# Kernel optimization log

Measured on AMD Instinct MI355X. Metric: run time of the kernel, lower is better.

## Reference

```python
import jax, jax.numpy as jnp
import numpy as np

N_QUMODES = 128
N_LAYERS = 8
BATCH = 131072
HBAR = 2.0  # PennyLane default.gaussian convention; vacuum covariance = I


def setup_inputs() -> dict:
    key = jax.random.key(0)
    k1, k2 = jax.random.split(key)
    inputs = jax.random.normal(k1, (BATCH, N_QUMODES), dtype=jnp.float32)
    params = jax.random.normal(k2, (N_LAYERS, 3 * N_QUMODES), dtype=jnp.float32)
    return {"inputs": inputs, "params": params}


def _rot(theta):
    # Rotation gate on (x, p): x -> c x - s p, p -> s x + c p. Shape [..., 2, 2].
    c, s = jnp.cos(theta), jnp.sin(theta)
    return jnp.stack([jnp.stack([c, -s], -1), jnp.stack([s, c], -1)], -2)


def _build_symplectic(params):
    """Compose the full 2N x 2N symplectic matrix for all layers.

    Per layer: local per-mode blocks R(th2) @ Sq(r) @ R(th1), then a fixed
    chain of pi/4 beamsplitters on modes (0,1),(1,2),...  Quadrature ordering
    is interleaved: (x0, p0, x1, p1, ...).
    """
    N, L = N_QUMODES, N_LAYERS
    p = params.reshape(L, N, 3)
    th1, r, th2 = p[..., 0], p[..., 1], p[..., 2]
    z = jnp.zeros_like(r)
    sq = jnp.stack([jnp.stack([jnp.exp(-r), z], -1),
                    jnp.stack([z, jnp.exp(r)], -1)], -2)  # [L, N, 2, 2]
    blk = jnp.einsum('lnab,lnbc,lncd->lnad', _rot(th2), sq, _rot(th1))

    # Fixed beamsplitter chain matrix C (theta = pi/4, phi = 0).
    t = float(np.cos(np.pi / 4))
    rr = float(np.sin(np.pi / 4))
    BS4 = jnp.array([[t, 0., -rr, 0.],
                     [0., t, 0., -rr],
                     [rr, 0., t, 0.],
                     [0., rr, 0., t]], dtype=params.dtype)
    C = jnp.eye(2 * N, dtype=params.dtype)
    for i in range(N - 1):
        C = C.at[2 * i:2 * i + 4, :].set(BS4 @ C[2 * i:2 * i + 4, :])

    idx = jnp.arange(N)
    S = jnp.eye(2 * N, dtype=params.dtype)
    for l in range(L):
        D = jnp.zeros((N, 2, N, 2), params.dtype).at[idx, :, idx, :].set(blk[l])
        S = C @ (D.reshape(2 * N, 2 * N) @ S)
    return S


def reference(inputs, params):
    """Batched Gaussian simulation of the CV QNN; returns <n_i> per sample."""
    S = _build_symplectic(params)
    B, N = inputs.shape[0], N_QUMODES
    # Displacement(a, 0): mu_x += sqrt(2*hbar) * a = 2a for hbar = 2.
    mu0 = jnp.zeros((B, 2 * N), inputs.dtype).at[:, 0::2].set(2.0 * inputs)
    mu = mu0 @ S.T                      # [B, 2N]
    V = S @ S.T                         # vacuum cov = I -> V = S S^T
    dV = jnp.diagonal(V)
    dsum = dV[0::2] + dV[1::2]          # V_xx + V_pp per mode, [N]
    n = (dsum[None, :] + mu[:, 0::2] ** 2 + mu[:, 1::2] ** 2) / (2.0 * HBAR) - 0.5
    return n
```

## Files before the change

kernel.cpp:

```cpp
#include <hip/hip_runtime.h>


#define BATCH 131072
#define PSTR 40

typedef __attribute__((ext_vector_type(8))) short bf16x8;
typedef __attribute__((ext_vector_type(4))) float f32x4;

#define MFMA(a, b, c) __builtin_amdgcn_mfma_f32_16x16x32_bf16(a, b, c, 0, 0, 0)

__device__ __forceinline__ unsigned short f2bf(float f) {
  unsigned int u = __float_as_uint(f);
  u += 0x7FFFu + ((u >> 16) & 1u);
  return (unsigned short)(u >> 16);
}
__device__ __forceinline__ float bf2f(unsigned short h) {
  return __uint_as_float(((unsigned int)h) << 16);
}
__device__ __forceinline__ void pack8(const float* v, uint4& hv, uint4& lv) {
  unsigned int hw[4], lw[4];
#pragma unroll
  for (int p = 0; p < 4; ++p) {
    unsigned short h0 = f2bf(v[2 * p]), h1 = f2bf(v[2 * p + 1]);
    unsigned short l0 = f2bf(v[2 * p] - bf2f(h0)), l1 = f2bf(v[2 * p + 1] - bf2f(h1));
    hw[p] = (unsigned int)h0 | ((unsigned int)h1 << 16);
    lw[p] = (unsigned int)l0 | ((unsigned int)l1 << 16);
  }
  hv = make_uint4(hw[0], hw[1], hw[2], hw[3]);
  lv = make_uint4(lw[0], lw[1], lw[2], lw[3]);
}

__device__ __forceinline__ float cxf(const float* powc, int a, int nn) {
  if (a < 127) {
    if (nn == 0) return powc[a + 1];
    if (nn <= a) return powc[a - nn + 2];
    if (nn == a + 1) return -0.70710678118654752f;
    return 0.0f;
  }
  return (nn == 0) ? powc[127] : powc[128 - nn];
}

__global__ __launch_bounds__(256) void l1_prod(const float* __restrict__ params,
                                               unsigned short* __restrict__ Phi,
                                               unsigned short* __restrict__ Plo) {
  __shared__ __align__(16) char lds_raw[4 * 128 * PSTR * 2];
  __shared__ float blkA[128][4];
  __shared__ float blkB[128][4];
  __shared__ float powc[132];
  unsigned short* sLhi = (unsigned short*)lds_raw;
  unsigned short* sLlo = sLhi + 128 * PSTR;
  unsigned short* sRhi = sLlo + 128 * PSTR;
  unsigned short* sRlo = sRhi + 128 * PSTR;
  float* sEp = (float*)lds_raw;

  int bx = blockIdx.x;
  int pair = bx >> 2, tile = bx & 3;
  int tr = tile >> 1, tc = tile & 1;
  int t = threadIdx.x;
  int lane = t & 63, w = t >> 6;
  int wr = (w >> 1) * 64, wc = (w & 1) * 64;
  int l15 = lane & 15, q = lane >> 4;

  {
    int l = (t < 128) ? (2 * pair + 1) : (2 * pair);
    int nn = t & 127;
    const float* p = params + l * 384 + nn * 3;
    float th1 = p[0], r = p[1], th2 = p[2];
    float c1 = cosf(th1), s1 = sinf(th1);
    float c2 = cosf(th2), s2 = sinf(th2);
    float em = expf(-r), ep = expf(r);
    float* dst = (t < 128) ? blkA[nn] : blkB[nn];
    dst[0] = c2 * c1 * em - s2 * s1 * ep;
    dst[1] = -c2 * s1 * em - s2 * c1 * ep;
    dst[2] = s2 * c1 * em + c2 * s1 * ep;
    dst[3] = -s2 * s1 * em + c2 * c1 * ep;
    if (t < 132) powc[t] = exp2f(-0.5f * (float)t);
  }

  f32x4 acc[4][4];
#pragma unroll
  for (int a = 0; a < 4; ++a)
#pragma unroll
    for (int b = 0; b < 4; ++b) acc[a][b] = (f32x4){0.f, 0.f, 0.f, 0.f};

  for (int kc = 0; kc < 256; kc += 32) {
    __syncthreads();
#pragma unroll
    for (int it = 0; it < 2; ++it) {
      int e = it * 2048 + t * 8;
      int row = e >> 5, k0 = e & 31;
      {
        int i = tr * 128 + row;
        int a = i >> 1;
        float vv[8];
#pragma unroll
        for (int jj = 0; jj < 8; ++jj) {
          int j = kc + k0 + jj;
          int nn = j >> 1;
          vv[jj] = cxf(powc, a, nn) * blkA[nn][(i & 1) * 2 + (j & 1)];
        }
        uint4 hv, lv;
        pack8(vv, hv, lv);
        *(uint4*)(sLhi + row * PSTR + k0) = hv;
        *(uint4*)(sLlo + row * PSTR + k0) = lv;
      }
      {
        int j = tc * 128 + row;
        int nn = j >> 1;
        float b0 = blkB[nn][0 + (j & 1)];
        float b1 = blkB[nn][2 + (j & 1)];
        float vv[8];
#pragma unroll
        for (int jj = 0; jj < 8; ++jj) {
          int i = kc + k0 + jj;
          vv[jj] = cxf(powc, i >> 1, nn) * ((i & 1) ? b1 : b0);
        }
        uint4 hv, lv;
        pack8(vv, hv, lv);
        *(uint4*)(sRhi + row * PSTR + k0) = hv;
        *(uint4*)(sRlo + row * PSTR + k0) = lv;
      }
    }
    __syncthreads();
    int kb = q * 8;
    bf16x8 afh[4], afl[4], bfh[4], bfl[4];
#pragma unroll
    for (int rt = 0; rt < 4; ++rt) {
      int r = wr + rt * 16 + l15;
      afh[rt] = *(const bf16x8*)(sLhi + r * PSTR + kb);
      afl[rt] = *(const bf16x8*)(sLlo + r * PSTR + kb);
      int n = wc + rt * 16 + l15;
      bfh[rt] = *(const bf16x8*)(sRhi + n * PSTR + kb);
      bfl[rt] = *(const bf16x8*)(sRlo + n * PSTR + kb);
    }
#pragma unroll
    for (int rt = 0; rt < 4; ++rt)
#pragma unroll
      for (int ct = 0; ct < 4; ++ct) {
        acc[rt][ct] = MFMA(afh[rt], bfh[ct], acc[rt][ct]);
        acc[rt][ct] = MFMA(afh[rt], bfl[ct], acc[rt][ct]);
        acc[rt][ct] = MFMA(afl[rt], bfh[ct], acc[rt][ct]);
      }
  }

  for (int ph = 0; ph < 2; ++ph) {
    __syncthreads();
    if (wr == ph * 64) {
#pragma unroll
      for (int rt = 0; rt < 4; ++rt)
#pragma unroll
        for (int ct = 0; ct < 4; ++ct) {
          int rl = rt * 16 + q * 4;
          int col = wc + ct * 16 + l15;
#pragma unroll
          for (int rg = 0; rg < 4; ++rg) sEp[(rl + rg) * 129 + col] = acc[rt][ct][rg];
        }
    }
    __syncthreads();
    if (pair & 1) {
      int rl = t >> 2, cseg = (t & 3) * 32;
      for (int cc = 0; cc < 32; cc += 8) {
        float v[8];
#pragma unroll
        for (int jj = 0; jj < 8; ++jj) v[jj] = sEp[rl * 129 + cseg + cc + jj];
        uint4 hv, lv;
        pack8(v, hv, lv);
        int off = pair * 65536 + (tr * 128 + ph * 64 + rl) * 256 + tc * 128 + cseg + cc;
        *(uint4*)(Phi + off) = hv;
        *(uint4*)(Plo + off) = lv;
      }
    } else {
      int col = t >> 1, rseg = (t & 1) * 32;
      for (int cc = 0; cc < 32; cc += 8) {
        float v[8];
#pragma unroll
        for (int jj = 0; jj < 8; ++jj) v[jj] = sEp[(rseg + cc + jj) * 129 + col];
        uint4 hv, lv;
        pack8(v, hv, lv);
        int off = pair * 65536 + (tc * 128 + col) * 256 + tr * 128 + ph * 64 + rseg + cc;
        *(uint4*)(Phi + off) = hv;
        *(uint4*)(Plo + off) = lv;
      }
    }
  }
}

__global__ __launch_bounds__(256) void matprod(
    const unsigned short* __restrict__ Lhi_base, const unsigned short* __restrict__ Llo_base,
    unsigned short* __restrict__ Ohi, unsigned short* __restrict__ Olo) {
  __shared__ __align__(16) char lds_raw[4 * 128 * PSTR * 2];
  unsigned short* sLhi = (unsigned short*)lds_raw;
  unsigned short* sLlo = sLhi + 128 * PSTR;
  unsigned short* sRhi = sLlo + 128 * PSTR;
  unsigned short* sRlo = sRhi + 128 * PSTR;
  float* sEp = (float*)lds_raw;

  int bx = blockIdx.x;
  int pair = bx >> 2, tile = bx & 3;
  int tr = tile >> 1, tc = tile & 1;
  const unsigned short* Lhi = Lhi_base + (2 * pair + 1) * 65536;
  const unsigned short* Llo = Llo_base + (2 * pair + 1) * 65536;
  const unsigned short* Rhi = Lhi_base + (2 * pair) * 65536;
  const unsigned short* Rlo = Llo_base + (2 * pair) * 65536;

  int t = threadIdx.x;
  int lane = t & 63, w = t >> 6;
  int wr = (w >> 1) * 64, wc = (w & 1) * 64;
  int l15 = lane & 15, q = lane >> 4;

  f32x4 acc[4][4];
#pragma unroll
  for (int a = 0; a < 4; ++a)
#pragma unroll
    for (int b = 0; b < 4; ++b) acc[a][b] = (f32x4){0.f, 0.f, 0.f, 0.f};

  for (int kc = 0; kc < 256; kc += 32) {
    __syncthreads();
#pragma unroll
    for (int it = 0; it < 2; ++it) {
      int e = it * 2048 + t * 8;
      int row = e >> 5, k = e & 31;
      *(uint4*)(sLhi + row * PSTR + k) = *(const uint4*)(Lhi + (tr * 128 + row) * 256 + kc + k);
      *(uint4*)(sLlo + row * PSTR + k) = *(const uint4*)(Llo + (tr * 128 + row) * 256 + kc + k);
      *(uint4*)(sRhi + row * PSTR + k) = *(const uint4*)(Rhi + (tc * 128 + row) * 256 + kc + k);
      *(uint4*)(sRlo + row * PSTR + k) = *(const uint4*)(Rlo + (tc * 128 + row) * 256 + kc + k);
    }
    __syncthreads();
    int kb = q * 8;
    bf16x8 afh[4], afl[4], bfh[4], bfl[4];
#pragma unroll
    for (int rt = 0; rt < 4; ++rt) {
      int r = wr + rt * 16 + l15;
      afh[rt] = *(const bf16x8*)(sLhi + r * PSTR + kb);
      afl[rt] = *(const bf16x8*)(sLlo + r * PSTR + kb);
      int n = wc + rt * 16 + l15;
      bfh[rt] = *(const bf16x8*)(sRhi + n * PSTR + kb);
      bfl[rt] = *(const bf16x8*)(sRlo + n * PSTR + kb);
    }
#pragma unroll
    for (int rt = 0; rt < 4; ++rt)
#pragma unroll
      for (int ct = 0; ct < 4; ++ct) {
        acc[rt][ct] = MFMA(afh[rt], bfh[ct], acc[rt][ct]);
        acc[rt][ct] = MFMA(afh[rt], bfl[ct], acc[rt][ct]);
        acc[rt][ct] = MFMA(afl[rt], bfh[ct], acc[rt][ct]);
      }
  }

  for (int ph = 0; ph < 2; ++ph) {
    __syncthreads();
    if (wr == ph * 64) {
#pragma unroll
      for (int rt = 0; rt < 4; ++rt)
#pragma unroll
        for (int ct = 0; ct < 4; ++ct) {
          int rl = rt * 16 + q * 4;
          int col = wc + ct * 16 + l15;
#pragma unroll
          for (int rg = 0; rg < 4; ++rg) sEp[(rl + rg) * 129 + col] = acc[rt][ct][rg];
        }
    }
    __syncthreads();
    if (pair & 1) {
      int rl = t >> 2, cseg = (t & 3) * 32;
      for (int cc = 0; cc < 32; cc += 8) {
        float v[8];
#pragma unroll
        for (int jj = 0; jj < 8; ++jj) v[jj] = sEp[rl * 129 + cseg + cc + jj];
        uint4 hv, lv;
        pack8(v, hv, lv);
        int off = pair * 65536 + (tr * 128 + ph * 64 + rl) * 256 + tc * 128 + cseg + cc;
        *(uint4*)(Ohi + off) = hv;
        *(uint4*)(Olo + off) = lv;
      }
    } else {
      int col = t >> 1, rseg = (t & 1) * 32;
      for (int cc = 0; cc < 32; cc += 8) {
        float v[8];
#pragma unroll
        for (int jj = 0; jj < 8; ++jj) v[jj] = sEp[(rseg + cc + jj) * 129 + col];
        uint4 hv, lv;
        pack8(v, hv, lv);
        int off = pair * 65536 + (tc * 128 + col) * 256 + tr * 128 + ph * 64 + rseg + cc;
        *(uint4*)(Ohi + off) = hv;
        *(uint4*)(Olo + off) = lv;
      }
    }
  }
}

__global__ __launch_bounds__(256) void l3_fused(
    const unsigned short* __restrict__ Qhi, const unsigned short* __restrict__ Qlo,
    unsigned short* __restrict__ Wb, float* __restrict__ dsum_part) {
  __shared__ __align__(16) char lds_raw[4 * 128 * PSTR * 2];
  unsigned short* sLhi = (unsigned short*)lds_raw;
  unsigned short* sLlo = sLhi + 128 * PSTR;
  unsigned short* sRhi = sLlo + 128 * PSTR;
  unsigned short* sRlo = sRhi + 128 * PSTR;
  float* sEp = (float*)lds_raw;

  int tile = blockIdx.x & 3;
  int tr = tile >> 1, tc = tile & 1;
  const unsigned short* Lhi = Qhi + 65536;
  const unsigned short* Llo = Qlo + 65536;
  const unsigned short* Rhi = Qhi;
  const unsigned short* Rlo = Qlo;

  int t = threadIdx.x;
  int lane = t & 63, w = t >> 6;
  int wr = (w >> 1) * 64, wc = (w & 1) * 64;
  int l15 = lane & 15, q = lane >> 4;

  f32x4 acc[4][4];
#pragma unroll
  for (int a = 0; a < 4; ++a)
#pragma unroll
    for (int b = 0; b < 4; ++b) acc[a][b] = (f32x4){0.f, 0.f, 0.f, 0.f};

  for (int kc = 0; kc < 256; kc += 32) {
    __syncthreads();
#pragma unroll
    for (int it = 0; it < 2; ++it) {
      int e = it * 2048 + t * 8;
      int row = e >> 5, k = e & 31;
      *(uint4*)(sLhi + row * PSTR + k) = *(const uint4*)(Lhi + (tr * 128 + row) * 256 + kc + k);
      *(uint4*)(sLlo + row * PSTR + k) = *(const uint4*)(Llo + (tr * 128 + row) * 256 + kc + k);
      *(uint4*)(sRhi + row * PSTR + k) = *(const uint4*)(Rhi + (tc * 128 + row) * 256 + kc + k);
      *(uint4*)(sRlo + row * PSTR + k) = *(const uint4*)(Rlo + (tc * 128 + row) * 256 + kc + k);
    }
    __syncthreads();
    int kb = q * 8;
    bf16x8 afh[4], afl[4], bfh[4], bfl[4];
#pragma unroll
    for (int rt = 0; rt < 4; ++rt) {
      int r = wr + rt * 16 + l15;
      afh[rt] = *(const bf16x8*)(sLhi + r * PSTR + kb);
      afl[rt] = *(const bf16x8*)(sLlo + r * PSTR + kb);
      int n = wc + rt * 16 + l15;
      bfh[rt] = *(const bf16x8*)(sRhi + n * PSTR + kb);
      bfl[rt] = *(const bf16x8*)(sRlo + n * PSTR + kb);
    }
#pragma unroll
    for (int rt = 0; rt < 4; ++rt)
#pragma unroll
      for (int ct = 0; ct < 4; ++ct) {
        acc[rt][ct] = MFMA(afh[rt], bfh[ct], acc[rt][ct]);
        acc[rt][ct] = MFMA(afh[rt], bfl[ct], acc[rt][ct]);
        acc[rt][ct] = MFMA(afl[rt], bfh[ct], acc[rt][ct]);
      }
  }

  for (int ph = 0; ph < 2; ++ph) {
    __syncthreads();
    if (wr == ph * 64) {
#pragma unroll
      for (int rt = 0; rt < 4; ++rt)
#pragma unroll
        for (int ct = 0; ct < 4; ++ct) {
          int rl = rt * 16 + q * 4;
          int col = wc + ct * 16 + l15;
#pragma unroll
          for (int rg = 0; rg < 4; ++rg) sEp[(rl + rg) * 129 + col] = acc[rt][ct][rg];
        }
    }
    __syncthreads();
    int rbase = tr * 128 + ph * 64;
    int ctbase = tr * 4 + ph * 2;
#pragma unroll
    for (int ci = 0; ci < 2; ++ci) {
      int cell = w * 2 + ci;
      int c2 = cell >> 1;
      int ct = ctbase + (c2 & 1) + ((c2 & 2) ? 8 : 0);
      int ks = 2 * tc + (cell & 1);
      int n = ct * 16 + l15;
      int srow = (n < 128) ? (2 * n) : (2 * (n - 128) + 1);
      int lr = srow - rbase;
      int lc0 = (cell & 1) * 64 + q * 16;
      float v[8];
#pragma unroll
      for (int jj = 0; jj < 8; ++jj) v[jj] = 2.0f * sEp[lr * 129 + lc0 + 2 * jj];
      unsigned int wd[4];
#pragma unroll
      for (int p2 = 0; p2 < 4; ++p2)
        wd[p2] = (unsigned int)f2bf(v[2 * p2]) | ((unsigned int)f2bf(v[2 * p2 + 1]) << 16);
      *(uint4*)(Wb + ((ct * 4 + ks) * 64 + lane) * 8) = make_uint4(wd[0], wd[1], wd[2], wd[3]);
    }
    {
      int ii = t >> 3, s = t & 7;
      int c0 = s * 16;
      float sum = 0.f;
#pragma unroll
      for (int c = 0; c < 16; ++c) {
        float x = sEp[(2 * ii) * 129 + c0 + c];
        float y = sEp[(2 * ii + 1) * 129 + c0 + c];
        sum += x * x + y * y;
      }
      sum += __shfl_down(sum, 4, 8);
      sum += __shfl_down(sum, 2, 8);
      sum += __shfl_down(sum, 1, 8);
      if (s == 0) dsum_part[tc * 128 + (rbase >> 1) + ii] = sum;
    }
  }
}

__global__ __launch_bounds__(256) void qnn_gemm(
    const float* __restrict__ A, const unsigned short* __restrict__ Wb,
    const float* __restrict__ dsum_part, float* __restrict__ out) {
  __shared__ unsigned short sA[64 * 136];
  int t = threadIdx.x;
  int lane = t & 63, w = t >> 6;
  int wr = w >> 1, wc = w & 1;
  int l15 = lane & 15, q = lane >> 4;
  long brow0 = (long)blockIdx.x * 64;

#pragma unroll
  for (int it = 0; it < 8; ++it) {
    int e = it * 1024 + t * 4;
    int row = e >> 7, k = e & 127;
    f32x4 v = __builtin_nontemporal_load((const f32x4*)(A + brow0 * 128 + e));
    *(uint2*)(sA + row * 136 + k) = make_uint2(
        (unsigned int)f2bf(v.x) | ((unsigned int)f2bf(v.y) << 16),
        (unsigned int)f2bf(v.z) | ((unsigned int)f2bf(v.w) << 16));
  }
  __syncthreads();

  f32x4 acc[2][4][2];
#pragma unroll
  for (int rt = 0; rt < 2; ++rt)
#pragma unroll
    for (int qq = 0; qq < 4; ++qq)
#pragma unroll
      for (int xp = 0; xp < 2; ++xp) acc[rt][qq][xp] = (f32x4){0.f, 0.f, 0.f, 0.f};

#pragma unroll
  for (int ks = 0; ks < 4; ++ks) {
    int kb = ks * 32 + q * 8;
    bf16x8 a0 = *(const bf16x8*)(sA + (wr * 32 + l15) * 136 + kb);
    bf16x8 a1 = *(const bf16x8*)(sA + (wr * 32 + 16 + l15) * 136 + kb);
#pragma unroll
    for (int qq = 0; qq < 4; ++qq)
#pragma unroll
      for (int xp = 0; xp < 2; ++xp) {
        int ct = wc * 4 + qq + 8 * xp;
        bf16x8 b = *(const bf16x8*)(Wb + ((ct * 4 + ks) * 64 + lane) * 8);
        acc[0][qq][xp] = MFMA(a0, b, acc[0][qq][xp]);
        acc[1][qq][xp] = MFMA(a1, b, acc[1][qq][xp]);
      }
  }

#pragma unroll
  for (int qq = 0; qq < 4; ++qq) {
    int i = (wc * 4 + qq) * 16 + l15;
    float ds = dsum_part[i] + dsum_part[128 + i];
#pragma unroll
    for (int rt = 0; rt < 2; ++rt) {
      long row0 = brow0 + wr * 32 + rt * 16 + q * 4;
      f32x4 ax = acc[rt][qq][0];
      f32x4 ap = acc[rt][qq][1];
#pragma unroll
      for (int rg = 0; rg < 4; ++rg) {
        float val = 0.25f * (ds + ax[rg] * ax[rg] + ap[rg] * ap[rg]) - 0.5f;
        __builtin_nontemporal_store(val, &out[(row0 + rg) * 128 + i]);
      }
    }
  }
}

extern "C" void kernel_launch(void* const* d_in, const int* in_sizes, int n_in,
                              void* d_out, int out_size, void* d_ws, size_t ws_size,
                              hipStream_t stream) {
  const float* inputs = (const float*)d_in[0];
  const float* params = (const float*)d_in[1];
  float* out = (float*)d_out;

  unsigned short* Phi = (unsigned short*)d_ws;
  unsigned short* Plo = Phi + 4 * 65536;
  unsigned short* Qhi = Plo + 4 * 65536;
  unsigned short* Qlo = Qhi + 2 * 65536;
  unsigned short* Wb = Qlo + 2 * 65536;
  float* dsum_part = (float*)(Wb + 65536);

  l1_prod<<<16, 256, 0, stream>>>(params, Phi, Plo);
  matprod<<<8, 256, 0, stream>>>(Phi, Plo, Qhi, Qlo);
  l3_fused<<<4, 256, 0, stream>>>(Qhi, Qlo, Wb, dsum_part);
  qnn_gemm<<<2048, 256, 0, stream>>>(inputs, Wb, dsum_part, out);
}
```

Before: 184.2 us.

## Make GEMM blocks persistent over four row chunks with register-prefetched double buffer

Each block of the batched GEMM now processes four 64-row chunks instead of one. The next chunk's fp32 inputs are loaded into registers while the current chunk's MFMAs run, then converted into a second LDS buffer. The dsum loads are hoisted out of the chunk loop, and the output stores switch from nontemporal to regular stores. The aim is to hide global load latency and amortize per-block setup, at the cost of a quarter as many blocks, fewer waves in flight, and more registers.

New measurement: 175.3 us. 1.05x faster.

```diff
diff --git a/kernel.cpp b/kernel.cpp
--- a/kernel.cpp
+++ b/kernel.cpp
@@ -403,65 +403,102 @@
   }
 }
 
+#define NCH 4
 __global__ __launch_bounds__(256) void qnn_gemm(
     const float* __restrict__ A, const unsigned short* __restrict__ Wb,
     const float* __restrict__ dsum_part, float* __restrict__ out) {
-  __shared__ unsigned short sA[64 * 136];
+  __shared__ unsigned short sA[2][64 * 136];
   int t = threadIdx.x;
   int lane = t & 63, w = t >> 6;
   int wr = w >> 1, wc = w & 1;
   int l15 = lane & 15, q = lane >> 4;
-  long brow0 = (long)blockIdx.x * 64;
-
+  long chunk0 = (long)blockIdx.x * NCH;
+
+  float ds[4];
+#pragma unroll
+  for (int qq = 0; qq < 4; ++qq) {
+    int i = (wc * 4 + qq) * 16 + l15;
+    ds[qq] = dsum_part[i] + dsum_part[128 + i];
+  }
+
+  f32x4 regs[8];
+#pragma unroll
+  for (int it = 0; it < 8; ++it)
+    regs[it] = __builtin_nontemporal_load((const f32x4*)(A + chunk0 * 8192 + it * 1024 + t * 4));
 #pragma unroll
   for (int it = 0; it < 8; ++it) {
     int e = it * 1024 + t * 4;
     int row = e >> 7, k = e & 127;
-    f32x4 v = __builtin_nontemporal_load((const f32x4*)(A + brow0 * 128 + e));
-    *(uint2*)(sA + row * 136 + k) = make_uint2(
+    f32x4 v = regs[it];
+    *(uint2*)(&sA[0][row * 136 + k]) = make_uint2(
         (unsigned int)f2bf(v.x) | ((unsigned int)f2bf(v.y) << 16),
         (unsigned int)f2bf(v.z) | ((unsigned int)f2bf(v.w) << 16));
   }
   __syncthreads();
 
-  f32x4 acc[2][4][2];
-#pragma unroll
-  for (int rt = 0; rt < 2; ++rt)
-#pragma unroll
-    for (int qq = 0; qq < 4; ++qq)
-#pragma unroll
-      for (int xp = 0; xp < 2; ++xp) acc[rt][qq][xp] = (f32x4){0.f, 0.f, 0.f, 0.f};
-
-#pragma unroll
-  for (int ks = 0; ks < 4; ++ks) {
-    int kb = ks * 32 + q * 8;
-    bf16x8 a0 = *(const bf16x8*)(sA + (wr * 32 + l15) * 136 + kb);
-    bf16x8 a1 = *(const bf16x8*)(sA + (wr * 32 + 16 + l15) * 136 + kb);
-#pragma unroll
-    for (int qq = 0; qq < 4; ++qq)
-#pragma unroll
-      for (int xp = 0; xp < 2; ++xp) {
-        int ct = wc * 4 + qq + 8 * xp;
-        bf16x8 b = *(const bf16x8*)(Wb + ((ct * 4 + ks) * 64 + lane) * 8);
-        acc[0][qq][xp] = MFMA(a0, b, acc[0][qq][xp]);
-        acc[1][qq][xp] = MFMA(a1, b, acc[1][qq][xp]);
-      }
-  }
-
-#pragma unroll
-  for (int qq = 0; qq < 4; ++qq) {
-    int i = (wc * 4 + qq) * 16 + l15;
-    float ds = dsum_part[i] + dsum_part[128 + i];
-#pragma unroll
-    for (int rt = 0; rt < 2; ++rt) {
-      long row0 = brow0 + wr * 32 + rt * 16 + q * 4;
-      f32x4 ax = acc[rt][qq][0];
-      f32x4 ap = acc[rt][qq][1];
-#pragma unroll
-      for (int rg = 0; rg < 4; ++rg) {
-        float val = 0.25f * (ds + ax[rg] * ax[rg] + ap[rg] * ap[rg]) - 0.5f;
-        __builtin_nontemporal_store(val, &out[(row0 + rg) * 128 + i]);
-      }
+#pragma unroll 1
+  for (int c = 0; c < NCH; ++c) {
+    int buf = c & 1;
+    long brow0 = (chunk0 + c) * 64;
+
+    if (c + 1 < NCH) {
+#pragma unroll
+      for (int it = 0; it < 8; ++it)
+        regs[it] = __builtin_nontemporal_load(
+            (const f32x4*)(A + (chunk0 + c + 1) * 8192 + it * 1024 + t * 4));
+    }
+
+    f32x4 acc[2][4][2];
+#pragma unroll
+    for (int rt = 0; rt < 2; ++rt)
+#pragma unroll
+      for (int qq = 0; qq < 4; ++qq)
+#pragma unroll
+        for (int xp = 0; xp < 2; ++xp) acc[rt][qq][xp] = (f32x4){0.f, 0.f, 0.f, 0.f};
+
+#pragma unroll
+    for (int ks = 0; ks < 4; ++ks) {
+      int kb = ks * 32 + q * 8;
+      bf16x8 a0 = *(const bf16x8*)(&sA[buf][(wr * 32 + l15) * 136 + kb]);
+      bf16x8 a1 = *(const bf16x8*)(&sA[buf][(wr * 32 + 16 + l15) * 136 + kb]);
+#pragma unroll
+      for (int qq = 0; qq < 4; ++qq)
+#pragma unroll
+        for (int xp = 0; xp < 2; ++xp) {
+          int ct = wc * 4 + qq + 8 * xp;
+          bf16x8 b = *(const bf16x8*)(Wb + ((ct * 4 + ks) * 64 + lane) * 8);
+          acc[0][qq][xp] = MFMA(a0, b, acc[0][qq][xp]);
+          acc[1][qq][xp] = MFMA(a1, b, acc[1][qq][xp]);
+        }
+    }
+
+#pragma unroll
+    for (int qq = 0; qq < 4; ++qq) {
+      int i = (wc * 4 + qq) * 16 + l15;
+#pragma unroll
+      for (int rt = 0; rt < 2; ++rt) {
+        long row0 = brow0 + wr * 32 + rt * 16 + q * 4;
+        f32x4 ax = acc[rt][qq][0];
+        f32x4 ap = acc[rt][qq][1];
+#pragma unroll
+        for (int rg = 0; rg < 4; ++rg) {
+          out[(row0 + rg) * 128 + i] =
+              0.25f * (ds[qq] + ax[rg] * ax[rg] + ap[rg] * ap[rg]) - 0.5f;
+        }
+      }
+    }
+
+    if (c + 1 < NCH) {
+#pragma unroll
+      for (int it = 0; it < 8; ++it) {
+        int e = it * 1024 + t * 4;
+        int row = e >> 7, k = e & 127;
+        f32x4 v = regs[it];
+        *(uint2*)(&sA[buf ^ 1][row * 136 + k]) = make_uint2(
+            (unsigned int)f2bf(v.x) | ((unsigned int)f2bf(v.y) << 16),
+            (unsigned int)f2bf(v.z) | ((unsigned int)f2bf(v.w) << 16));
+      }
+      __syncthreads();
     }
   }
 }
@@ -483,5 +520,5 @@
   l1_prod<<<16, 256, 0, stream>>>(params, Phi, Plo);
   matprod<<<8, 256, 0, stream>>>(Phi, Plo, Qhi, Qlo);
   l3_fused<<<4, 256, 0, stream>>>(Qhi, Qlo, Wb, dsum_part);
-  qnn_gemm<<<2048, 256, 0, stream>>>(inputs, Wb, dsum_part, out);
-}
+  qnn_gemm<<<BATCH / (64 * NCH), 256, 0, stream>>>(inputs, Wb, dsum_part, out);
+}
```
